# Kernel tuning notes

Measured on AMD Instinct MI355X. Metric: run time of the kernel, lower is better.

## Reference

```python
import jax, jax.numpy as jnp
import numpy as np

D_MODEL = 512
D_VALUE = 512
N_HEADS = 8
NEG_INF = -1e30


def _layernorm(x, g, b, eps=1e-5):
    mu = jnp.mean(x, axis=-1, keepdims=True)
    var = jnp.var(x, axis=-1, keepdims=True)
    return (x - mu) * jax.lax.rsqrt(var + eps) * g + b


def setup_inputs() -> dict:
    key = jax.random.key(0)
    ks = jax.random.split(key, 16)
    B, L, dq = 4, 2048, 512
    d_model, d_value, H = D_MODEL, D_VALUE, N_HEADS
    d4 = 4 * d_model
    s = lambda d: 1.0 / np.sqrt(d)
    inp = {
        "q": jax.random.normal(ks[0], (B, L, dq), jnp.float32),
        "k": jax.random.normal(ks[1], (B, L, dq), jnp.float32),
        "v": jax.random.normal(ks[2], (B, L, d_value), jnp.float32),
        "Wq": jax.random.normal(ks[3], (d_model, dq), jnp.float32) * s(dq),
        "bq": jnp.zeros((d_model,), jnp.float32),
        "Wk": jax.random.normal(ks[4], (d_model, dq), jnp.float32) * s(dq),
        "bk": jnp.zeros((d_model,), jnp.float32),
        "Wv": jax.random.normal(ks[5], (d_model, d_value), jnp.float32) * s(d_value),
        "bv": jnp.zeros((d_model,), jnp.float32),
        "Wo": jax.random.normal(ks[6], (d_value, d_model), jnp.float32) * s(d_model),
        "bo": jnp.zeros((d_value,), jnp.float32),
        "Wc1": jax.random.normal(ks[7], (d4, d_value), jnp.float32) * s(d_value),
        "bc1": jnp.zeros((d4,), jnp.float32),
        "Wc2": jax.random.normal(ks[8], (d_value, d4), jnp.float32) * s(d4),
        "bc2": jnp.zeros((d_value,), jnp.float32),
        "g1": jnp.ones((d_value,), jnp.float32),
        "b1": jnp.zeros((d_value,), jnp.float32),
        "g2": jnp.ones((d_value,), jnp.float32),
        "b2": jnp.zeros((d_value,), jnp.float32),
        "Wl": jax.random.normal(ks[9], (d_model, d_value), jnp.float32) * s(d_value),
        "bl": jnp.zeros((d_model,), jnp.float32),
    }
    return inp


def reference(q, k, v, Wq, bq, Wk, bk, Wv, bv, Wo, bo, Wc1, bc1, Wc2, bc2,
              g1, b1, g2, b2, Wl, bl):
    B, L, _ = q.shape
    S = k.shape[1]
    H = N_HEADS
    E = D_MODEL // H
    # projections -> [B, L, H, E]
    queries = (q @ Wq.T + bq).reshape(B, L, H, E)
    keys = (k @ Wk.T + bk).reshape(B, S, H, E)
    values = (v @ Wv.T + bv).reshape(B, S, H, E)
    # naive causal attention, full [B,H,L,S] scores
    scale = 1.0 / np.sqrt(E)
    scores = jnp.einsum('blhe,bshe->bhls', queries, keys)
    causal = jnp.triu(jnp.ones((L, S), dtype=bool), k=1)  # True above diagonal
    scores = jnp.where(causal, NEG_INF, scores)
    A = jax.nn.softmax(scale * scores, axis=-1)
    att = jnp.einsum('bhls,bshd->blhd', A, values).reshape(B, L, H * E)
    att = att @ Wo.T + bo
    # residual + FFN (conv1d kernel_size=1 == pointwise linear)
    x = _layernorm(v + att, g1, b1)
    y = jax.nn.relu(x @ Wc1.T + bc1)
    y = y @ Wc2.T + bc2
    y = _layernorm(x + y, g2, b2)
    return y @ Wl.T + bl
```

## Files before the change

kernel.cpp:

```cpp
#include <hip/hip_runtime.h>
#include <hip/hip_bf16.h>


typedef __attribute__((ext_vector_type(8))) short sh8;
typedef __attribute__((ext_vector_type(4))) float f32x4;

#define QSCALE 0.18033688011110543f

__device__ __forceinline__ void storeOut(float* p, float v) { *p = v; }
__device__ __forceinline__ void storeOut(__hip_bfloat16* p, float v) { *p = __float2bfloat16(v); }

__device__ __forceinline__ void gl_lds16(const void* g, void* l) {
    __builtin_amdgcn_global_load_lds((const __attribute__((address_space(1))) void*)g,
                                     (__attribute__((address_space(3))) void*)l, 16, 0, 0);
}

__device__ __forceinline__ unsigned pk_bf16(float a, float b) {
    __hip_bfloat162 h = __float22bfloat162_rn(make_float2(a, b));
    return *(unsigned*)&h;
}
__device__ __forceinline__ float bf2f(unsigned short u) {
    unsigned x = (unsigned)u << 16;
    return *(float*)&x;
}

struct WArg { const float* w[7]; unsigned short* wd; };
__global__ __launch_bounds__(256) void conv_w(WArg p)
{
    const int i = (blockIdx.x * 256 + threadIdx.x) * 4;
    if (i >= 3407872) return;
    const float* s; int off;
    if      (i < 262144)  { s = p.w[0]; off = i; }
    else if (i < 524288)  { s = p.w[1]; off = i - 262144; }
    else if (i < 786432)  { s = p.w[2]; off = i - 524288; }
    else if (i < 1048576) { s = p.w[3]; off = i - 786432; }
    else if (i < 1310720) { s = p.w[4]; off = i - 1048576; }
    else if (i < 2359296) { s = p.w[5]; off = i - 1310720; }
    else                  { s = p.w[6]; off = i - 2359296; }
    const float4 v = *(const float4*)(s + off);
    *(uint2*)(p.wd + i) = make_uint2(pk_bf16(v.x, v.y), pk_bf16(v.z, v.w));
}

__global__ __launch_bounds__(256) void conv_in(const float* __restrict__ q,
                                               const float* __restrict__ k,
                                               const float* __restrict__ v,
                                               unsigned short* __restrict__ dst)
{
    const int i = (blockIdx.x * 256 + threadIdx.x) * 4;
    if (i >= 12582912) return;
    const float* s; int off;
    if      (i < 4194304) { s = q; off = i; }
    else if (i < 8388608) { s = k; off = i - 4194304; }
    else                  { s = v; off = i - 8388608; }
    const float4 x = *(const float4*)(s + off);
    *(uint2*)(dst + i) = make_uint2(pk_bf16(x.x, x.y), pk_bf16(x.z, x.w));
}

struct QkvArg {
    const unsigned short *A0, *A1, *A2;
    const float *b0, *b1, *b2;
    unsigned short *C0, *C1;
    unsigned short *Vt;
};
__global__ __launch_bounds__(256, 2) void gemm_qkv(QkvArg ar, const unsigned short* __restrict__ Wall,
                                                   int M, int N, int K)
{
    const int z = blockIdx.z;
    const unsigned short* A = z == 0 ? ar.A0 : (z == 1 ? ar.A1 : ar.A2);
    const unsigned short* W = Wall + (size_t)z * 262144;
    const float* bias = z == 0 ? ar.b0 : (z == 1 ? ar.b1 : ar.b2);

    __shared__ unsigned short AsL[2][8192];
    __shared__ unsigned short BsL[2][8192];
    const int t    = threadIdx.x;
    const int wave = t >> 6, lane = t & 63;
    const int quad = lane >> 4, col = lane & 15;
    const int wm   = wave >> 1, wn = wave & 1;
    const int m0   = blockIdx.y * 128, n0 = blockIdx.x * 128;

    auto stage = [&](int k0, int buf) {
        #pragma unroll
        for (int seg = 0; seg < 4; seg++) {
            const int r0  = (seg * 4 + wave) * 8;
            const int row = r0 + (lane >> 3);
            const int ck  = (lane & 7) ^ (row & 7);
            gl_lds16(A + (size_t)(m0 + row) * K + k0 + ck * 8, &AsL[buf][r0 * 64]);
            gl_lds16(W + (size_t)(n0 + row) * K + k0 + ck * 8, &BsL[buf][r0 * 64]);
        }
    };

    f32x4 acc[4][4];
    #pragma unroll
    for (int mt = 0; mt < 4; mt++)
        #pragma unroll
        for (int nt = 0; nt < 4; nt++)
            acc[mt][nt] = (f32x4){0.f, 0.f, 0.f, 0.f};

    stage(0, 0);
    __syncthreads();
    int cur = 0;
    for (int k0 = 0; k0 < K; k0 += 64) {
        if (k0 + 64 < K) stage(k0 + 64, cur ^ 1);
        #pragma unroll
        for (int kc = 0; kc < 2; kc++) {
            sh8 af[4], bf[4];
            #pragma unroll
            for (int mt = 0; mt < 4; mt++) {
                const int arow = wm * 64 + mt * 16 + col;
                af[mt] = *(const sh8*)&AsL[cur][arow * 64 + (((kc * 4 + quad) ^ (arow & 7)) << 3)];
            }
            #pragma unroll
            for (int nt = 0; nt < 4; nt++) {
                const int nr = wn * 64 + nt * 16 + col;
                bf[nt] = *(const sh8*)&BsL[cur][nr * 64 + (((kc * 4 + quad) ^ (nr & 7)) << 3)];
            }
            #pragma unroll
            for (int mt = 0; mt < 4; mt++)
                #pragma unroll
                for (int nt = 0; nt < 4; nt++)
                    acc[mt][nt] = __builtin_amdgcn_mfma_f32_16x16x32_bf16(af[mt], bf[nt], acc[mt][nt], 0, 0, 0);
        }
        __syncthreads();
        cur ^= 1;
    }

    if (z < 2) {
        unsigned short* C = z == 0 ? ar.C0 : ar.C1;
        const float scale = z == 0 ? QSCALE : 1.0f;
        #pragma unroll
        for (int nt = 0; nt < 4; nt++) {
            const int cn = n0 + wn * 64 + nt * 16 + col;
            const float bj = bias[cn];
            #pragma unroll
            for (int mt = 0; mt < 4; mt++) {
                const int rm = m0 + wm * 64 + mt * 16 + quad * 4;
                #pragma unroll
                for (int reg = 0; reg < 4; reg++)
                    C[(size_t)(rm + reg) * N + cn] =
                        (unsigned short)__bfloat16_as_ushort(__float2bfloat16((acc[mt][nt][reg] + bj) * scale));
            }
        }
    } else {
        const int b = m0 >> 11;
        #pragma unroll
        for (int nt = 0; nt < 4; nt++) {
            const int cn = n0 + wn * 64 + nt * 16 + col;
            const int h = cn >> 6, e = cn & 63;
            const float bj = bias[cn];
            #pragma unroll
            for (int mt = 0; mt < 4; mt++) {
                const int s0r = (m0 + wm * 64 + mt * 16 + quad * 4) & 2047;
                float cv[4];
                #pragma unroll
                for (int reg = 0; reg < 4; reg++) cv[reg] = acc[mt][nt][reg] + bj;
                *(uint2*)(ar.Vt + ((size_t)(b * 8 + h) * 64 + e) * 2048 + s0r) =
                    make_uint2(pk_bf16(cv[0], cv[1]), pk_bf16(cv[2], cv[3]));
            }
        }
    }
}

template <typename TOUT, bool RELU>
__global__ __launch_bounds__(256, 2) void gemm_mfma(const unsigned short* __restrict__ A,
                                                    const unsigned short* __restrict__ W,
                                                    const float* __restrict__ bias,
                                                    TOUT* __restrict__ C,
                                                    int M, int N, int K)
{
    __shared__ unsigned short AsL[2][8192];
    __shared__ unsigned short BsL[2][8192];
    const int t    = threadIdx.x;
    const int wave = t >> 6, lane = t & 63;
    const int quad = lane >> 4, col = lane & 15;
    const int wm   = wave >> 1, wn = wave & 1;
    const int m0   = blockIdx.y * 128, n0 = blockIdx.x * 128;

    auto stage = [&](int k0, int buf) {
        #pragma unroll
        for (int seg = 0; seg < 4; seg++) {
            const int r0  = (seg * 4 + wave) * 8;
            const int row = r0 + (lane >> 3);
            const int ck  = (lane & 7) ^ (row & 7);
            gl_lds16(A + (size_t)(m0 + row) * K + k0 + ck * 8, &AsL[buf][r0 * 64]);
            gl_lds16(W + (size_t)(n0 + row) * K + k0 + ck * 8, &BsL[buf][r0 * 64]);
        }
    };

    f32x4 acc[4][4];
    #pragma unroll
    for (int mt = 0; mt < 4; mt++)
        #pragma unroll
        for (int nt = 0; nt < 4; nt++)
            acc[mt][nt] = (f32x4){0.f, 0.f, 0.f, 0.f};

    stage(0, 0);
    __syncthreads();
    int cur = 0;
    for (int k0 = 0; k0 < K; k0 += 64) {
        if (k0 + 64 < K) stage(k0 + 64, cur ^ 1);
        #pragma unroll
        for (int kc = 0; kc < 2; kc++) {
            sh8 af[4], bf[4];
            #pragma unroll
            for (int mt = 0; mt < 4; mt++) {
                const int ar = wm * 64 + mt * 16 + col;
                af[mt] = *(const sh8*)&AsL[cur][ar * 64 + (((kc * 4 + quad) ^ (ar & 7)) << 3)];
            }
            #pragma unroll
            for (int nt = 0; nt < 4; nt++) {
                const int nr = wn * 64 + nt * 16 + col;
                bf[nt] = *(const sh8*)&BsL[cur][nr * 64 + (((kc * 4 + quad) ^ (nr & 7)) << 3)];
            }
            #pragma unroll
            for (int mt = 0; mt < 4; mt++)
                #pragma unroll
                for (int nt = 0; nt < 4; nt++)
                    acc[mt][nt] = __builtin_amdgcn_mfma_f32_16x16x32_bf16(af[mt], bf[nt], acc[mt][nt], 0, 0, 0);
        }
        __syncthreads();
        cur ^= 1;
    }
    #pragma unroll
    for (int nt = 0; nt < 4; nt++) {
        const int cn = n0 + wn * 64 + nt * 16 + col;
        const float bj = bias[cn];
        #pragma unroll
        for (int mt = 0; mt < 4; mt++) {
            const int rm = m0 + wm * 64 + mt * 16 + quad * 4;
            #pragma unroll
            for (int reg = 0; reg < 4; reg++) {
                float cv = acc[mt][nt][reg] + bj;
                if (RELU) cv = fmaxf(cv, 0.f);
                storeOut(&C[(size_t)(rm + reg) * N + cn], cv);
            }
        }
    }
}

template <typename TOUT, bool RELU>
__global__ __launch_bounds__(256, 2) void gemm_mfma64(const unsigned short* __restrict__ A,
                                                      const unsigned short* __restrict__ W,
                                                      const float* __restrict__ bias,
                                                      TOUT* __restrict__ C,
                                                      int M, int N, int K)
{
    __shared__ unsigned short AsL[2][4096];
    __shared__ unsigned short BsL[2][8192];
    const int t    = threadIdx.x;
    const int wave = t >> 6, lane = t & 63;
    const int quad = lane >> 4, col = lane & 15;
    const int wm   = wave >> 1, wn = wave & 1;
    const int m0   = blockIdx.y * 64, n0 = blockIdx.x * 128;

    auto stage = [&](int k0, int buf) {
        #pragma unroll
        for (int seg = 0; seg < 2; seg++) {
            const int r0  = (seg * 4 + wave) * 8;
            const int row = r0 + (lane >> 3);
            const int ck  = (lane & 7) ^ (row & 7);
            gl_lds16(A + (size_t)(m0 + row) * K + k0 + ck * 8, &AsL[buf][r0 * 64]);
        }
        #pragma unroll
        for (int seg = 0; seg < 4; seg++) {
            const int r0  = (seg * 4 + wave) * 8;
            const int row = r0 + (lane >> 3);
            const int ck  = (lane & 7) ^ (row & 7);
            gl_lds16(W + (size_t)(n0 + row) * K + k0 + ck * 8, &BsL[buf][r0 * 64]);
        }
    };

    f32x4 acc[2][4];
    #pragma unroll
    for (int mt = 0; mt < 2; mt++)
        #pragma unroll
        for (int nt = 0; nt < 4; nt++)
            acc[mt][nt] = (f32x4){0.f, 0.f, 0.f, 0.f};

    stage(0, 0);
    __syncthreads();
    int cur = 0;
    for (int k0 = 0; k0 < K; k0 += 64) {
        if (k0 + 64 < K) stage(k0 + 64, cur ^ 1);
        #pragma unroll
        for (int kc = 0; kc < 2; kc++) {
            sh8 af[2], bf[4];
            #pragma unroll
            for (int mt = 0; mt < 2; mt++) {
                const int ar = wm * 32 + mt * 16 + col;
                af[mt] = *(const sh8*)&AsL[cur][ar * 64 + (((kc * 4 + quad) ^ (ar & 7)) << 3)];
            }
            #pragma unroll
            for (int nt = 0; nt < 4; nt++) {
                const int nr = wn * 64 + nt * 16 + col;
                bf[nt] = *(const sh8*)&BsL[cur][nr * 64 + (((kc * 4 + quad) ^ (nr & 7)) << 3)];
            }
            #pragma unroll
            for (int mt = 0; mt < 2; mt++)
                #pragma unroll
                for (int nt = 0; nt < 4; nt++)
                    acc[mt][nt] = __builtin_amdgcn_mfma_f32_16x16x32_bf16(af[mt], bf[nt], acc[mt][nt], 0, 0, 0);
        }
        __syncthreads();
        cur ^= 1;
    }
    #pragma unroll
    for (int nt = 0; nt < 4; nt++) {
        const int cn = n0 + wn * 64 + nt * 16 + col;
        const float bj = bias[cn];
        #pragma unroll
        for (int mt = 0; mt < 2; mt++) {
            const int rm = m0 + wm * 32 + mt * 16 + quad * 4;
            #pragma unroll
            for (int reg = 0; reg < 4; reg++) {
                float cv = acc[mt][nt][reg] + bj;
                if (RELU) cv = fmaxf(cv, 0.f);
                storeOut(&C[(size_t)(rm + reg) * N + cn], cv);
            }
        }
    }
}

__global__ __launch_bounds__(256, 2) void attn_mfma(const unsigned short* __restrict__ Qb,
                                                    const unsigned short* __restrict__ Kb,
                                                    const unsigned short* __restrict__ Vt,
                                                    __hip_bfloat16* __restrict__ O,
                                                    int L)
{
    __shared__ unsigned short Ks[2][4096];
    __shared__ unsigned short Vs[2][4096];
    __shared__ unsigned short PsA[4][16][72];
    __shared__ unsigned short PsB[4][16][72];

    const int i    = blockIdx.x;
    const int bh   = blockIdx.y;
    const int b    = bh >> 3, h = bh & 7;
    const int t    = threadIdx.x;
    const int w    = t >> 6, lane = t & 63;
    const int quad = lane >> 4, col = lane & 15;

    const int qtA = i, qtB = 31 - i;
    const int qrowA = qtA * 64 + w * 16 + col;
    const int qrowB = qtB * 64 + w * 16 + col;
    const int S = 32 - i;

    const int srow = lane >> 3;
    const int scp  = lane & 7;

    sh8 qfA[2], qfB[2];
    {
        const size_t qa = ((size_t)(b * L + qrowA) * 8 + h) * 64;
        qfA[0] = *(const sh8*)(Qb + qa + quad * 8);
        qfA[1] = *(const sh8*)(Qb + qa + 32 + quad * 8);
        const size_t qb2 = ((size_t)(b * L + qrowB) * 8 + h) * 64;
        qfB[0] = *(const sh8*)(Qb + qb2 + quad * 8);
        qfB[1] = *(const sh8*)(Qb + qb2 + 32 + quad * 8);
    }

    f32x4 OA[4], OB[4];
    #pragma unroll
    for (int nt = 0; nt < 4; nt++) { OA[nt] = (f32x4){0.f,0.f,0.f,0.f}; OB[nt] = (f32x4){0.f,0.f,0.f,0.f}; }
    float lA = 0.f, lB = 0.f;

    {
        #pragma unroll
        for (int seg = 0; seg < 2; seg++) {
            const int r0  = (seg * 4 + w) * 8;
            const int row = r0 + srow;
            const int ck  = scp ^ (row & 7);
            gl_lds16(Kb + ((size_t)(b * L + row) * 8 + h) * 64 + ck * 8, &Ks[0][r0 * 64]);
            gl_lds16(Vt + (size_t)(bh * 64 + row) * L + ck * 8, &Vs[0][r0 * 64]);
        }
        __syncthreads();
    }

    int cur = 0;
    for (int r = 0; r < S; r++) {
        if (r + 1 < S) {
            const int k1 = (r + 1) * 64;
            #pragma unroll
            for (int seg = 0; seg < 2; seg++) {
                const int r0  = (seg * 4 + w) * 8;
                const int row = r0 + srow;
                const int ck  = scp ^ (row & 7);
                gl_lds16(Kb + ((size_t)(b * L + k1 + row) * 8 + h) * 64 + ck * 8, &Ks[cur ^ 1][r0 * 64]);
                gl_lds16(Vt + (size_t)(bh * 64 + row) * L + k1 + ck * 8, &Vs[cur ^ 1][r0 * 64]);
            }
        }

        const int k0 = r * 64;
        const bool actA  = (r <= i);
        const bool maskA = (r == i);
        const bool maskB = (r == S - 1);

        f32x4 stA[4], stB[4];
        const f32x4 zz = {0.f, 0.f, 0.f, 0.f};
        #pragma unroll
        for (int ntk = 0; ntk < 4; ntk++) {
            const int key = ntk * 16 + col;
            const int sw  = key & 7;
            sh8 kf0 = *(const sh8*)&Ks[cur][key * 64 + ((quad ^ sw) << 3)];
            sh8 kf1 = *(const sh8*)&Ks[cur][key * 64 + (((quad + 4) ^ sw) << 3)];
            f32x4 aB = __builtin_amdgcn_mfma_f32_16x16x32_bf16(kf0, qfB[0], zz, 0, 0, 0);
            stB[ntk] = __builtin_amdgcn_mfma_f32_16x16x32_bf16(kf1, qfB[1], aB, 0, 0, 0);
            if (actA) {
                f32x4 aA = __builtin_amdgcn_mfma_f32_16x16x32_bf16(kf0, qfA[0], zz, 0, 0, 0);
                stA[ntk] = __builtin_amdgcn_mfma_f32_16x16x32_bf16(kf1, qfA[1], aA, 0, 0, 0);
            }
        }

        {
            if (maskB) {
                #pragma unroll
                for (int ntk = 0; ntk < 4; ntk++)
                    #pragma unroll
                    for (int reg = 0; reg < 4; reg++)
                        if (k0 + ntk * 16 + quad * 4 + reg > qrowB) stB[ntk][reg] = -1e30f;
            }
            #pragma unroll
            for (int ntk = 0; ntk < 4; ntk++) {
                #pragma unroll
                for (int reg = 0; reg < 4; reg++)
                    stB[ntk][reg] = exp2f(stB[ntk][reg]);
                lB += (stB[ntk][0] + stB[ntk][1]) + (stB[ntk][2] + stB[ntk][3]);
                *(uint2*)&PsB[w][col][ntk * 16 + quad * 4] =
                    make_uint2(pk_bf16(stB[ntk][0], stB[ntk][1]), pk_bf16(stB[ntk][2], stB[ntk][3]));
            }
        }
        if (actA) {
            if (maskA) {
                #pragma unroll
                for (int ntk = 0; ntk < 4; ntk++)
                    #pragma unroll
                    for (int reg = 0; reg < 4; reg++)
                        if (k0 + ntk * 16 + quad * 4 + reg > qrowA) stA[ntk][reg] = -1e30f;
            }
            #pragma unroll
            for (int ntk = 0; ntk < 4; ntk++) {
                #pragma unroll
                for (int reg = 0; reg < 4; reg++)
                    stA[ntk][reg] = exp2f(stA[ntk][reg]);
                lA += (stA[ntk][0] + stA[ntk][1]) + (stA[ntk][2] + stA[ntk][3]);
                *(uint2*)&PsA[w][col][ntk * 16 + quad * 4] =
                    make_uint2(pk_bf16(stA[ntk][0], stA[ntk][1]), pk_bf16(stA[ntk][2], stA[ntk][3]));
            }
        }

        #pragma unroll
        for (int kchunk = 0; kchunk < 2; kchunk++) {
            sh8 pfB = *(const sh8*)&PsB[w][col][kchunk * 32 + quad * 8];
            sh8 pfA;
            if (actA) pfA = *(const sh8*)&PsA[w][col][kchunk * 32 + quad * 8];
            #pragma unroll
            for (int nt = 0; nt < 4; nt++) {
                const int e  = nt * 16 + col;
                sh8 vf = *(const sh8*)&Vs[cur][e * 64 + (((kchunk * 4 + quad) ^ (e & 7)) << 3)];
                OB[nt] = __builtin_amdgcn_mfma_f32_16x16x32_bf16(pfB, vf, OB[nt], 0, 0, 0);
                if (actA) OA[nt] = __builtin_amdgcn_mfma_f32_16x16x32_bf16(pfA, vf, OA[nt], 0, 0, 0);
            }
        }
        __syncthreads();
        cur ^= 1;
    }

    lA += __shfl_xor(lA, 16); lA += __shfl_xor(lA, 32);
    lB += __shfl_xor(lB, 16); lB += __shfl_xor(lB, 32);
    {
        const float li = 1.f / lA;
        float lr[4];
        #pragma unroll
        for (int reg = 0; reg < 4; reg++) lr[reg] = __shfl(li, quad * 4 + reg);
        #pragma unroll
        for (int reg = 0; reg < 4; reg++) {
            const int qr = qtA * 64 + w * 16 + quad * 4 + reg;
            #pragma unroll
            for (int nt = 0; nt < 4; nt++)
                O[((size_t)(b * L + qr) * 8 + h) * 64 + nt * 16 + col] =
                    __float2bfloat16(OA[nt][reg] * lr[reg]);
        }
    }
    {
        const float li = 1.f / lB;
        float lr[4];
        #pragma unroll
        for (int reg = 0; reg < 4; reg++) lr[reg] = __shfl(li, quad * 4 + reg);
        #pragma unroll
        for (int reg = 0; reg < 4; reg++) {
            const int qr = qtB * 64 + w * 16 + quad * 4 + reg;
            #pragma unroll
            for (int nt = 0; nt < 4; nt++)
                O[((size_t)(b * L + qr) * 8 + h) * 64 + nt * 16 + col] =
                    __float2bfloat16(OB[nt][reg] * lr[reg]);
        }
    }
}

__global__ __launch_bounds__(256) void layernorm_k(const unsigned short* __restrict__ f1,
                                                   const unsigned short* __restrict__ f2,
                                                   const float* __restrict__ rb,
                                                   const float* __restrict__ g,
                                                   const float* __restrict__ bb,
                                                   unsigned short* __restrict__ out16)
{
    const int row = blockIdx.x;
    const int t   = threadIdx.x;
    const size_t base = (size_t)row * 512;
    const int i0 = t * 2;

    const unsigned u1 = *(const unsigned*)(f1 + base + i0);
    float a0 = bf2f((unsigned short)(u1 & 0xffff));
    float a1 = bf2f((unsigned short)(u1 >> 16));
    if (f2) {
        const unsigned u2 = *(const unsigned*)(f2 + base + i0);
        a0 += bf2f((unsigned short)(u2 & 0xffff));
        a1 += bf2f((unsigned short)(u2 >> 16));
    }
    if (rb) { a0 += rb[base + i0]; a1 += rb[base + i0 + 1]; }

    float s = a0 + a1, ss = a0 * a0 + a1 * a1;
    #pragma unroll
    for (int off = 32; off > 0; off >>= 1) {
        s  += __shfl_xor(s, off);
        ss += __shfl_xor(ss, off);
    }
    __shared__ float red[16];
    const int lane = t & 63, wid = t >> 6;
    if (lane == 0) { red[wid] = s; red[8 + wid] = ss; }
    __syncthreads();
    if (t == 0) {
        const float S  = red[0] + red[1] + red[2] + red[3];
        const float SS = red[8] + red[9] + red[10] + red[11];
        const float mu = S * (1.f / 512.f);
        const float var = SS * (1.f / 512.f) - mu * mu;
        red[0] = mu;
        red[1] = rsqrtf(fmaxf(var, 0.f) + 1e-5f);
    }
    __syncthreads();
    const float mu = red[0], rstd = red[1];
    const float y0 = (a0 - mu) * rstd * g[i0]     + bb[i0];
    const float y1 = (a1 - mu) * rstd * g[i0 + 1] + bb[i0 + 1];
    *(unsigned*)(out16 + base + i0) = pk_bf16(y0, y1);
}

extern "C" void kernel_launch(void* const* d_in, const int* in_sizes, int n_in,
                              void* d_out, int out_size, void* d_ws, size_t ws_size,
                              hipStream_t stream)
{
    const float* q   = (const float*)d_in[0];
    const float* k   = (const float*)d_in[1];
    const float* v   = (const float*)d_in[2];
    const float* Wq  = (const float*)d_in[3];
    const float* bq  = (const float*)d_in[4];
    const float* Wk  = (const float*)d_in[5];
    const float* bk  = (const float*)d_in[6];
    const float* Wv  = (const float*)d_in[7];
    const float* bv  = (const float*)d_in[8];
    const float* Wo  = (const float*)d_in[9];
    const float* bo  = (const float*)d_in[10];
    const float* Wc1 = (const float*)d_in[11];
    const float* bc1 = (const float*)d_in[12];
    const float* Wc2 = (const float*)d_in[13];
    const float* bc2 = (const float*)d_in[14];
    const float* g1  = (const float*)d_in[15];
    const float* b1  = (const float*)d_in[16];
    const float* g2  = (const float*)d_in[17];
    const float* b2  = (const float*)d_in[18];
    const float* Wl  = (const float*)d_in[19];
    const float* bl  = (const float*)d_in[20];
    float* out = (float*)d_out;

    const int B = 4, L = 2048, H = 8;
    const int M = B * L;

    char* base = (char*)d_ws;
    unsigned short* Wall = (unsigned short*)(base + 0);
    unsigned short* Wob  = (unsigned short*)(base + 1572864);
    unsigned short* Wlb  = (unsigned short*)(base + 2097152);
    unsigned short* Wc1b = (unsigned short*)(base + 2621440);
    unsigned short* Wc2b = (unsigned short*)(base + 4718592);
    unsigned short* Qb   = (unsigned short*)(base + 6815744);
    unsigned short* Kb   = (unsigned short*)(base + 15204352);
    unsigned short* Vt   = (unsigned short*)(base + 23592960);
    unsigned short* A1   = (unsigned short*)(base + 31981568);
    unsigned short* Ab   = (unsigned short*)(base + 40370176);
    unsigned short* A2b  = (unsigned short*)(base + 40370176);
    unsigned short* Y2b  = (unsigned short*)(base + 48758784);
    unsigned short* X1b  = (unsigned short*)(base + 73924608);
    unsigned short* X2b  = (unsigned short*)(base + 73924608);
    unsigned short* H1   = (unsigned short*)(base + 6815744);
    const dim3 blk(256);

    WArg wa;
    wa.w[0] = Wq; wa.w[1] = Wk; wa.w[2] = Wv; wa.w[3] = Wo; wa.w[4] = Wl;
    wa.w[5] = Wc1; wa.w[6] = Wc2; wa.wd = Wall;
    conv_w<<<dim3(3328), blk, 0, stream>>>(wa);

    conv_in<<<dim3(12288), blk, 0, stream>>>(q, k, v, Ab);

    QkvArg qa;
    qa.A0 = Ab; qa.A1 = Ab + 4194304; qa.A2 = Ab + 8388608;
    qa.b0 = bq; qa.b1 = bk; qa.b2 = bv;
    qa.C0 = Qb; qa.C1 = Kb; qa.Vt = Vt;
    gemm_qkv<<<dim3(4, 64, 3), blk, 0, stream>>>(qa, Wall, M, 512, 512);

    attn_mfma<<<dim3(16, B * H), blk, 0, stream>>>(Qb, Kb, Vt, (__hip_bfloat16*)A1, L);

    gemm_mfma64<__hip_bfloat16, false><<<dim3(4, 128), blk, 0, stream>>>(A1, Wob, bo, (__hip_bfloat16*)A2b, M, 512, 512);

    layernorm_k<<<dim3(M), blk, 0, stream>>>(A2b, nullptr, v, g1, b1, X1b);

    gemm_mfma<__hip_bfloat16, true><<<dim3(16, 64), blk, 0, stream>>>(X1b, Wc1b, bc1, (__hip_bfloat16*)H1, M, 2048, 512);

    gemm_mfma64<__hip_bfloat16, false><<<dim3(4, 128), blk, 0, stream>>>(H1, Wc2b, bc2, (__hip_bfloat16*)Y2b, M, 512, 2048);

    layernorm_k<<<dim3(M), blk, 0, stream>>>(X1b, Y2b, nullptr, g2, b2, X2b);

    gemm_mfma64<float, false><<<dim3(4, 128), blk, 0, stream>>>(X2b, Wlb, bl, out, M, 512, 512);
}
```

Before: 313.2 us.

## Fuse fp32-to-bf16 input conversion into QKV GEMM and swizzle GEMM block order

Drops the separate conv_in kernel. The QKV GEMM now loads fp32 q/k/v tiles straight into LDS and packs them to bf16 in registers before the MFMA, with the K-step cut from 64 to 32 so LDS usage stays the same. This removes a full read and write pass over the bf16 input copy. It also remaps block indices in the other GEMMs so that groups of consecutive blocks share weight and row tiles, aiming for better L2 reuse. The cost is more K-loop iterations with a sync each, plus pack instructions in the inner loop.

```diff
diff --git a/kernel.cpp b/kernel.cpp
--- a/kernel.cpp
+++ b/kernel.cpp
@@ -22,6 +22,11 @@
 __device__ __forceinline__ float bf2f(unsigned short u) {
     unsigned x = (unsigned)u << 16;
     return *(float*)&x;
+}
+__device__ __forceinline__ sh8 pk8(float4 a, float4 b) {
+    int4 iv = make_int4(pk_bf16(a.x, a.y), pk_bf16(a.z, a.w),
+                        pk_bf16(b.x, b.y), pk_bf16(b.z, b.w));
+    return *(sh8*)&iv;
 }
 
 struct WArg { const float* w[7]; unsigned short* wd; };
@@ -41,23 +46,8 @@
     *(uint2*)(p.wd + i) = make_uint2(pk_bf16(v.x, v.y), pk_bf16(v.z, v.w));
 }
 
-__global__ __launch_bounds__(256) void conv_in(const float* __restrict__ q,
-                                               const float* __restrict__ k,
-                                               const float* __restrict__ v,
-                                               unsigned short* __restrict__ dst)
-{
-    const int i = (blockIdx.x * 256 + threadIdx.x) * 4;
-    if (i >= 12582912) return;
-    const float* s; int off;
-    if      (i < 4194304) { s = q; off = i; }
-    else if (i < 8388608) { s = k; off = i - 4194304; }
-    else                  { s = v; off = i - 8388608; }
-    const float4 x = *(const float4*)(s + off);
-    *(uint2*)(dst + i) = make_uint2(pk_bf16(x.x, x.y), pk_bf16(x.z, x.w));
-}
-
 struct QkvArg {
-    const unsigned short *A0, *A1, *A2;
+    const float *A0, *A1, *A2;
     const float *b0, *b1, *b2;
     unsigned short *C0, *C1;
     unsigned short *Vt;
@@ -66,12 +56,12 @@
                                                    int M, int N, int K)
 {
     const int z = blockIdx.z;
-    const unsigned short* A = z == 0 ? ar.A0 : (z == 1 ? ar.A1 : ar.A2);
+    const float* A = z == 0 ? ar.A0 : (z == 1 ? ar.A1 : ar.A2);
     const unsigned short* W = Wall + (size_t)z * 262144;
     const float* bias = z == 0 ? ar.b0 : (z == 1 ? ar.b1 : ar.b2);
 
-    __shared__ unsigned short AsL[2][8192];
-    __shared__ unsigned short BsL[2][8192];
+    __shared__ float AsF[2][4096];
+    __shared__ unsigned short BsL[2][4096];
     const int t    = threadIdx.x;
     const int wave = t >> 6, lane = t & 63;
     const int quad = lane >> 4, col = lane & 15;
@@ -84,8 +74,14 @@
             const int r0  = (seg * 4 + wave) * 8;
             const int row = r0 + (lane >> 3);
             const int ck  = (lane & 7) ^ (row & 7);
-            gl_lds16(A + (size_t)(m0 + row) * K + k0 + ck * 8, &AsL[buf][r0 * 64]);
-            gl_lds16(W + (size_t)(n0 + row) * K + k0 + ck * 8, &BsL[buf][r0 * 64]);
+            gl_lds16(A + (size_t)(m0 + row) * K + k0 + ck * 4, &AsF[buf][r0 * 32]);
+        }
+        #pragma unroll
+        for (int seg = 0; seg < 2; seg++) {
+            const int r0  = (seg * 4 + wave) * 16;
+            const int row = r0 + (lane >> 2);
+            const int ck  = (lane & 3) ^ (row & 3);
+            gl_lds16(W + (size_t)(n0 + row) * K + k0 + ck * 8, &BsL[buf][r0 * 32]);
         }
     };
 
@@ -99,27 +95,28 @@
     stage(0, 0);
     __syncthreads();
     int cur = 0;
-    for (int k0 = 0; k0 < K; k0 += 64) {
-        if (k0 + 64 < K) stage(k0 + 64, cur ^ 1);
-        #pragma unroll
-        for (int kc = 0; kc < 2; kc++) {
-            sh8 af[4], bf[4];
-            #pragma unroll
-            for (int mt = 0; mt < 4; mt++) {
-                const int arow = wm * 64 + mt * 16 + col;
-                af[mt] = *(const sh8*)&AsL[cur][arow * 64 + (((kc * 4 + quad) ^ (arow & 7)) << 3)];
-            }
-            #pragma unroll
-            for (int nt = 0; nt < 4; nt++) {
-                const int nr = wn * 64 + nt * 16 + col;
-                bf[nt] = *(const sh8*)&BsL[cur][nr * 64 + (((kc * 4 + quad) ^ (nr & 7)) << 3)];
-            }
-            #pragma unroll
-            for (int mt = 0; mt < 4; mt++)
-                #pragma unroll
-                for (int nt = 0; nt < 4; nt++)
-                    acc[mt][nt] = __builtin_amdgcn_mfma_f32_16x16x32_bf16(af[mt], bf[nt], acc[mt][nt], 0, 0, 0);
-        }
+    for (int k0 = 0; k0 < K; k0 += 32) {
+        if (k0 + 32 < K) stage(k0 + 32, cur ^ 1);
+        sh8 af[4], bf[4];
+        #pragma unroll
+        for (int mt = 0; mt < 4; mt++) {
+            const int mr = wm * 64 + mt * 16 + col;
+            const int q0 = quad * 2;
+            const int m8 = mr & 7;
+            float4 f0 = *(const float4*)&AsF[cur][mr * 32 + ((q0 ^ m8) << 2)];
+            float4 f1 = *(const float4*)&AsF[cur][mr * 32 + (((q0 + 1) ^ m8) << 2)];
+            af[mt] = pk8(f0, f1);
+        }
+        #pragma unroll
+        for (int nt = 0; nt < 4; nt++) {
+            const int nr = wn * 64 + nt * 16 + col;
+            bf[nt] = *(const sh8*)&BsL[cur][nr * 32 + ((quad ^ (nr & 3)) << 3)];
+        }
+        #pragma unroll
+        for (int mt = 0; mt < 4; mt++)
+            #pragma unroll
+            for (int nt = 0; nt < 4; nt++)
+                acc[mt][nt] = __builtin_amdgcn_mfma_f32_16x16x32_bf16(af[mt], bf[nt], acc[mt][nt], 0, 0, 0);
         __syncthreads();
         cur ^= 1;
     }
@@ -173,7 +170,11 @@
     const int wave = t >> 6, lane = t & 63;
     const int quad = lane >> 4, col = lane & 15;
     const int wm   = wave >> 1, wn = wave & 1;
-    const int m0   = blockIdx.y * 128, n0 = blockIdx.x * 128;
+    const int NB  = gridDim.x, MB = gridDim.y;
+    const int lin = blockIdx.x + NB * blockIdx.y;
+    const int mi  = (lin & 7) * (MB >> 3) + (lin >> 3) / NB;
+    const int ni  = (lin >> 3) % NB;
+    const int m0  = mi * 128, n0 = ni * 128;
 
     auto stage = [&](int k0, int buf) {
         #pragma unroll
@@ -250,7 +251,11 @@
     const int wave = t >> 6, lane = t & 63;
     const int quad = lane >> 4, col = lane & 15;
     const int wm   = wave >> 1, wn = wave & 1;
-    const int m0   = blockIdx.y * 64, n0 = blockIdx.x * 128;
+    const int NB  = gridDim.x, MB = gridDim.y;
+    const int lin = blockIdx.x + NB * blockIdx.y;
+    const int mi  = (lin & 7) * (MB >> 3) + (lin >> 3) / NB;
+    const int ni  = (lin >> 3) % NB;
+    const int m0  = mi * 64, n0 = ni * 128;
 
     auto stage = [&](int k0, int buf) {
         #pragma unroll
@@ -581,7 +586,6 @@
     unsigned short* Kb   = (unsigned short*)(base + 15204352);
     unsigned short* Vt   = (unsigned short*)(base + 23592960);
     unsigned short* A1   = (unsigned short*)(base + 31981568);
-    unsigned short* Ab   = (unsigned short*)(base + 40370176);
     unsigned short* A2b  = (unsigned short*)(base + 40370176);
     unsigned short* Y2b  = (unsigned short*)(base + 48758784);
     unsigned short* X1b  = (unsigned short*)(base + 73924608);
@@ -594,10 +598,8 @@
     wa.w[5] = Wc1; wa.w[6] = Wc2; wa.wd = Wall;
     conv_w<<<dim3(3328), blk, 0, stream>>>(wa);
 
-    conv_in<<<dim3(12288), blk, 0, stream>>>(q, k, v, Ab);
-
     QkvArg qa;
-    qa.A0 = Ab; qa.A1 = Ab + 4194304; qa.A2 = Ab + 8388608;
+    qa.A0 = q;  qa.A1 = k;  qa.A2 = v;
     qa.b0 = bq; qa.b1 = bk; qa.b2 = bv;
     qa.C0 = Qb; qa.C1 = Kb; qa.Vt = Vt;
     gemm_qkv<<<dim3(4, 64, 3), blk, 0, stream>>>(qa, Wall, M, 512, 512);
```

Measured after the change: 308.9 us (median of 2 runs). Within noise of the previous version (-1.4%).
